# Kernel tuning notes

Measured on AMD Instinct MI355X. Metric: run time of the kernel, lower is better.

The kernel has to match this reference:

```python
import jax, jax.numpy as jnp
import numpy as np

S, B, E, H = 2048, 2, 1024, 16
D = E // H  # head_dim = 64


def setup_inputs() -> dict:
    key = jax.random.key(0)
    ks = jax.random.split(key, 5)
    sp = (2.0 / (E + E)) ** 0.5  # xavier-ish scale
    return {
        "x": jax.random.normal(ks[0], (S, B, E), dtype=jnp.float32),
        "wq": jax.random.normal(ks[1], (E, E), dtype=jnp.float32) * sp,
        "bq": jnp.zeros((E,), jnp.float32),
        "wk": jax.random.normal(ks[2], (E, E), dtype=jnp.float32) * sp,
        "bk": jnp.zeros((E,), jnp.float32),
        "wv": jax.random.normal(ks[3], (E, E), dtype=jnp.float32) * sp,
        "bv": jnp.zeros((E,), jnp.float32),
        "wo": jax.random.normal(ks[4], (E, E), dtype=jnp.float32) * sp,
        "bo": jnp.zeros((E,), jnp.float32),
    }


def reference(x, wq, bq, wk, bk, wv, bv, wo, bo):
    # x: (S, B, E), weights in torch Linear convention (out, in)
    scaling = jnp.float32(D ** -0.5)
    q = (jnp.einsum('ibe,fe->ibf', x, wq) + bq) * scaling
    k = jnp.einsum('ibe,fe->ibf', x, wk) + bk
    v = jnp.einsum('ibe,fe->ibf', x, wv) + bv
    q = q.reshape(S, B, H, D)
    k = k.reshape(S, B, H, D)
    v = v.reshape(S, B, H, D)
    # energy: (B, H, S_q, S_k)
    energy = jnp.einsum('ibnf,jbnf->bnij', q, k)
    causal = jnp.triu(jnp.ones((S, S), dtype=bool), k=1)  # True above diagonal
    energy = jnp.where(causal[None, None], -jnp.inf, energy)
    weights = jax.nn.softmax(energy, axis=-1)
    head_ctx = jnp.einsum('bnij,jbnf->ibnf', weights, v)
    context = head_ctx.reshape(S, B, E)
    out = jnp.einsum('ibe,fe->ibf', context, wo) + bo
    return out
```

## Files before the change

### kernel.cpp

```cpp
#include <hip/hip_runtime.h>
#include <hip/hip_bf16.h>
#include <stdint.h>

#define S_LEN 2048
#define BATCH 2
#define EMB   1024
#define NH    16
#define HD    64
#define LOG2E 1.4426950408889634f

typedef __bf16 bf16x8 __attribute__((ext_vector_type(8)));
typedef float  f32x4  __attribute__((ext_vector_type(4)));
typedef unsigned short ushort8 __attribute__((ext_vector_type(8)));

__device__ __forceinline__ unsigned short f2bf(float f) {
  __bf16 h = (__bf16)f;
  return __builtin_bit_cast(unsigned short, h);
}

__device__ __forceinline__ ushort8 cvt8(const float4 a, const float4 b) {
  ushort8 o;
  o[0]=f2bf(a.x); o[1]=f2bf(a.y); o[2]=f2bf(a.z); o[3]=f2bf(a.w);
  o[4]=f2bf(b.x); o[5]=f2bf(b.y); o[6]=f2bf(b.z); o[7]=f2bf(b.w);
  return o;
}

#define GLOAD16(g, l) __builtin_amdgcn_global_load_lds( \
    (const __attribute__((address_space(1))) void*)(g),  \
    (__attribute__((address_space(3))) void*)(l), 16, 0, 0)

__global__ __launch_bounds__(256) void k_cvt(const float* __restrict__ src,
                                             unsigned short* __restrict__ dst,
                                             int n) {
  int i = (blockIdx.x*256 + threadIdx.x)*8;
  if (i >= n) return;
  const float4* s4 = (const float4*)(src + i);
  *(ushort8*)(dst + i) = cvt8(s4[0], s4[1]);
}

__global__ __launch_bounds__(256) void k_qkv_bb(
    const unsigned short* __restrict__ xb,
    const unsigned short* __restrict__ wb,
    const float* __restrict__ bq, const float* __restrict__ bk,
    const float* __restrict__ bv,
    unsigned short* __restrict__ Qb, unsigned short* __restrict__ Kb,
    unsigned short* __restrict__ Vtb)
{
  __shared__ unsigned short Al[128*32];
  __shared__ unsigned short Bl[128*32];
  const int tid = threadIdx.x;
  const int lin  = blockIdx.x;
  const int wgid = (lin & 7)*96 + (lin >> 3);
  const int mb   = wgid / 24;
  const int t    = wgid % 24;
  const int z    = t >> 3;
  const int nb   = t & 7;
  const int m0 = mb * 128;
  const int n0 = nb * 128;
  const int w = tid >> 6, lane = tid & 63;
  const int wr = w >> 1, wc = w & 1;
  const int lr = lane & 15, lhi = lane >> 4;
  const unsigned short* wz = wb + (size_t)z * (EMB*EMB);

  f32x4 acc[4][4];
#pragma unroll
  for (int m=0;m<4;++m)
#pragma unroll
    for (int n=0;n<4;++n) acc[m][n] = (f32x4){0.f,0.f,0.f,0.f};

  for (int k0 = 0; k0 < EMB; k0 += 32) {
    __syncthreads();
#pragma unroll
    for (int j = 0; j < 2; ++j) {
      const int c   = j*256 + tid;
      const int row = c >> 2;
      const int col = (c & 3) << 3;
      const int ub  = (j*256 + (tid & 192)) * 16;
      GLOAD16(xb + (size_t)(m0+row)*EMB + k0 + col, (char*)Al + ub);
      GLOAD16(wz + (size_t)(n0+row)*EMB + k0 + col, (char*)Bl + ub);
    }
    __syncthreads();
    bf16x8 af[4], bfr[4];
#pragma unroll
    for (int m=0;m<4;++m) af[m]  = *(const bf16x8*)&Al[(wr*64 + m*16 + lr)*32 + lhi*8];
#pragma unroll
    for (int n=0;n<4;++n) bfr[n] = *(const bf16x8*)&Bl[(wc*64 + n*16 + lr)*32 + lhi*8];
#pragma unroll
    for (int m=0;m<4;++m)
#pragma unroll
      for (int n=0;n<4;++n)
        acc[m][n] = __builtin_amdgcn_mfma_f32_16x16x32_bf16(af[m], bfr[n], acc[m][n], 0,0,0);
  }

  const float scale = (z==0) ? 0.125f*LOG2E : 1.0f;
  const float* bias = (z==0) ? bq : ((z==1) ? bk : bv);
#pragma unroll
  for (int m=0;m<4;++m)
#pragma unroll
    for (int n=0;n<4;++n)
#pragma unroll
      for (int r=0;r<4;++r) {
        const int rr   = m0 + wr*64 + m*16 + lhi*4 + r;
        const int fcol = n0 + wc*64 + n*16 + lr;
        const float v = (acc[m][n][r] + bias[fcol]) * scale;
        const unsigned short ov = f2bf(v);
        const int i = rr >> 1, bsel = rr & 1;
        const int h = fcol >> 6, d = fcol & 63;
        const int hh = bsel*NH + h;
        if (z == 0)      Qb [((size_t)hh*S_LEN + i)*HD + d] = ov;
        else if (z == 1) Kb [((size_t)hh*S_LEN + i)*HD + d] = ov;
        else             Vtb[((size_t)hh*HD + d)*S_LEN + i] = ov;
      }
}

__global__ __launch_bounds__(256) void k_qkv_bf(
    const unsigned short* __restrict__ xb,
    const float* __restrict__ wq, const float* __restrict__ wk,
    const float* __restrict__ wv,
    const float* __restrict__ bq, const float* __restrict__ bk,
    const float* __restrict__ bv,
    unsigned short* __restrict__ Qb, unsigned short* __restrict__ Kb,
    unsigned short* __restrict__ Vtb)
{
  __shared__ unsigned short Al[128*32];
  __shared__ unsigned short Bl[128*32];
  const int tid = threadIdx.x;
  const int lin  = blockIdx.x;
  const int wgid = (lin & 7)*96 + (lin >> 3);
  const int mb   = wgid / 24;
  const int t    = wgid % 24;
  const int z    = t >> 3;
  const int nb   = t & 7;
  const int m0 = mb * 128;
  const int n0 = nb * 128;
  const int w = tid >> 6, lane = tid & 63;
  const int wr = w >> 1, wc = w & 1;
  const int lr = lane & 15, lhi = lane >> 4;
  const float* wz = (z==0) ? wq : ((z==1) ? wk : wv);

  f32x4 acc[4][4];
#pragma unroll
  for (int m=0;m<4;++m)
#pragma unroll
    for (int n=0;n<4;++n) acc[m][n] = (f32x4){0.f,0.f,0.f,0.f};

  for (int k0 = 0; k0 < EMB; k0 += 32) {
    float4 b0[2], b1[2];
#pragma unroll
    for (int j = 0; j < 2; ++j) {
      const int c   = j*256 + tid;
      const int row = c >> 2;
      const int col = (c & 3) << 3;
      const float* bp = wz + (size_t)(n0+row)*EMB + k0 + col;
      b0[j] = *(const float4*)bp;  b1[j] = *(const float4*)(bp+4);
    }
    __syncthreads();
#pragma unroll
    for (int j = 0; j < 2; ++j) {
      const int c   = j*256 + tid;
      const int row = c >> 2;
      const int col = (c & 3) << 3;
      const int ub  = (j*256 + (tid & 192)) * 16;
      GLOAD16(xb + (size_t)(m0+row)*EMB + k0 + col, (char*)Al + ub);
      *(ushort8*)&Bl[row*32 + col] = cvt8(b0[j], b1[j]);
    }
    __syncthreads();
    bf16x8 af[4], bfr[4];
#pragma unroll
    for (int m=0;m<4;++m) af[m]  = *(const bf16x8*)&Al[(wr*64 + m*16 + lr)*32 + lhi*8];
#pragma unroll
    for (int n=0;n<4;++n) bfr[n] = *(const bf16x8*)&Bl[(wc*64 + n*16 + lr)*32 + lhi*8];
#pragma unroll
    for (int m=0;m<4;++m)
#pragma unroll
      for (int n=0;n<4;++n)
        acc[m][n] = __builtin_amdgcn_mfma_f32_16x16x32_bf16(af[m], bfr[n], acc[m][n], 0,0,0);
  }

  const float scale = (z==0) ? 0.125f*LOG2E : 1.0f;
  const float* bias = (z==0) ? bq : ((z==1) ? bk : bv);
#pragma unroll
  for (int m=0;m<4;++m)
#pragma unroll
    for (int n=0;n<4;++n)
#pragma unroll
      for (int r=0;r<4;++r) {
        const int rr   = m0 + wr*64 + m*16 + lhi*4 + r;
        const int fcol = n0 + wc*64 + n*16 + lr;
        const float v = (acc[m][n][r] + bias[fcol]) * scale;
        const unsigned short ov = f2bf(v);
        const int i = rr >> 1, bsel = rr & 1;
        const int h = fcol >> 6, d = fcol & 63;
        const int hh = bsel*NH + h;
        if (z == 0)      Qb [((size_t)hh*S_LEN + i)*HD + d] = ov;
        else if (z == 1) Kb [((size_t)hh*S_LEN + i)*HD + d] = ov;
        else             Vtb[((size_t)hh*HD + d)*S_LEN + i] = ov;
      }
}

__global__ __launch_bounds__(256) void k_qkv(
    const float* __restrict__ xA, int a_rs, int ishift,
    const float* __restrict__ wq, const float* __restrict__ wk,
    const float* __restrict__ wv,
    const float* __restrict__ bq, const float* __restrict__ bk,
    const float* __restrict__ bv,
    unsigned short* __restrict__ Qb, unsigned short* __restrict__ Kb,
    unsigned short* __restrict__ Vtb)
{
  __shared__ unsigned short Al[128*32];
  __shared__ unsigned short Bl[128*32];
  const int tid = threadIdx.x;
  const int z  = blockIdx.z;
  const int m0 = blockIdx.x * 128;
  const int n0 = blockIdx.y * 128;
  const int w = tid >> 6, lane = tid & 63;
  const int wr = w >> 1, wc = w & 1;
  const int lr = lane & 15, lhi = lane >> 4;
  const float* wz = (z==0) ? wq : ((z==1) ? wk : wv);

  f32x4 acc[4][4];
#pragma unroll
  for (int m=0;m<4;++m)
#pragma unroll
    for (int n=0;n<4;++n) acc[m][n] = (f32x4){0.f,0.f,0.f,0.f};

  for (int k0 = 0; k0 < EMB; k0 += 32) {
    float4 a0[2], a1[2], b0[2], b1[2];
#pragma unroll
    for (int j = 0; j < 2; ++j) {
      const int c   = j*256 + tid;
      const int row = c >> 2;
      const int col = (c & 3) << 3;
      const float* ap = xA + (size_t)(m0+row)*a_rs + k0 + col;
      const float* bp = wz + (size_t)(n0+row)*EMB + k0 + col;
      a0[j] = *(const float4*)ap;  a1[j] = *(const float4*)(ap+4);
      b0[j] = *(const float4*)bp;  b1[j] = *(const float4*)(bp+4);
    }
    __syncthreads();
#pragma unroll
    for (int j = 0; j < 2; ++j) {
      const int c   = j*256 + tid;
      const int row = c >> 2;
      const int col = (c & 3) << 3;
      *(ushort8*)&Al[row*32 + col] = cvt8(a0[j], a1[j]);
      *(ushort8*)&Bl[row*32 + col] = cvt8(b0[j], b1[j]);
    }
    __syncthreads();
    bf16x8 af[4], bfr[4];
#pragma unroll
    for (int m=0;m<4;++m) af[m]  = *(const bf16x8*)&Al[(wr*64 + m*16 + lr)*32 + lhi*8];
#pragma unroll
    for (int n=0;n<4;++n) bfr[n] = *(const bf16x8*)&Bl[(wc*64 + n*16 + lr)*32 + lhi*8];
#pragma unroll
    for (int m=0;m<4;++m)
#pragma unroll
      for (int n=0;n<4;++n)
        acc[m][n] = __builtin_amdgcn_mfma_f32_16x16x32_bf16(af[m], bfr[n], acc[m][n], 0,0,0);
  }

  const float scale = (z==0) ? 0.125f*LOG2E : 1.0f;
  const float* bias = (z==0) ? bq : ((z==1) ? bk : bv);
  const int bmask = (1 << ishift) - 1;
#pragma unroll
  for (int m=0;m<4;++m)
#pragma unroll
    for (int n=0;n<4;++n)
#pragma unroll
      for (int r=0;r<4;++r) {
        const int rr   = m0 + wr*64 + m*16 + lhi*4 + r;
        const int fcol = n0 + wc*64 + n*16 + lr;
        const float v = (acc[m][n][r] + bias[fcol]) * scale;
        const unsigned short ov = f2bf(v);
        const int i = rr >> ishift, bsel = rr & bmask;
        const int h = fcol >> 6, d = fcol & 63;
        const int hh = bsel*NH + h;
        if (z == 0)      Qb [((size_t)hh*S_LEN + i)*HD + d] = ov;
        else if (z == 1) Kb [((size_t)hh*S_LEN + i)*HD + d] = ov;
        else             Vtb[((size_t)hh*HD + d)*S_LEN + i] = ov;
      }
}

__global__ __launch_bounds__(256,4) void k_attn(
    const unsigned short* __restrict__ Q,
    const unsigned short* __restrict__ K,
    const unsigned short* __restrict__ Vt,
    unsigned short* __restrict__ ctx, int bshift, int hsh)
{
  __shared__ unsigned short KL[2][64*64];
  __shared__ unsigned short VL[2][64*64];
  __shared__ unsigned short Pl[4][1024];

  const int tid = threadIdx.x;
  const int w = tid >> 6, lane = tid & 63;
  const int lr = lane & 15, lhi = lane >> 4;

  const int lin = blockIdx.x;
  const int cc  = lin >> hsh;
  const int chunk = (cc < 16) ? cc : (47 - cc);
  const int hh  = lin & ((1 << hsh) - 1);
  const int q0  = chunk*64 + w*16;

  const unsigned short* Qh = Q  + (size_t)hh*S_LEN*HD;
  const unsigned short* Kh = K  + (size_t)hh*S_LEN*HD;
  const unsigned short* Vh = Vt + (size_t)hh*HD*S_LEN;
  unsigned short* Pw = Pl[w];

  bf16x8 qf[2];
#pragma unroll
  for (int kf=0;kf<2;++kf)
    qf[kf] = *(const bf16x8*)&Qh[(size_t)(q0 + lr)*HD + kf*32 + lhi*8];

  f32x4 o[4];
  float rm = -3.0e38f, rl = 0.f;
#pragma unroll
  for (int dn=0;dn<4;++dn) o[dn] = (f32x4){0.f,0.f,0.f,0.f};

  const int tmax = chunk + 1;

  auto STAGE = [&](int tt, int bb2) {
    const int kv0 = tt*64;
#pragma unroll
    for (int j = 0; j < 2; ++j) {
      const int c   = j*256 + tid;
      const int row = c >> 3;
      const int sb  = (c*16) ^ ((row & 7) << 4);
      const int el  = (sb & 127) >> 1;
      const int ub  = (j*256 + (tid & 192)) * 16;
      GLOAD16(Kh + (size_t)(kv0+row)*HD + el,        (char*)KL[bb2] + ub);
      GLOAD16(Vh + (size_t)row*S_LEN + kv0 + el,     (char*)VL[bb2] + ub);
    }
  };

  STAGE(0, 0);
  int bb = 0;
  for (int t = 0; t < tmax; ++t) {
    if (t + 1 < tmax) {
      STAGE(t+1, bb^1);
      asm volatile("s_waitcnt vmcnt(4)" ::: "memory");
    } else {
      asm volatile("s_waitcnt vmcnt(0)" ::: "memory");
    }
    __builtin_amdgcn_s_barrier();

    const int kv0 = t*64;
    const char* KB = (const char*)KL[bb];
    const char* VB = (const char*)VL[bb];

    f32x4 st[4];
#pragma unroll
    for (int kn=0;kn<4;++kn) st[kn] = (f32x4){0.f,0.f,0.f,0.f};

    __builtin_amdgcn_s_setprio(1);
#pragma unroll
    for (int kn=0;kn<4;++kn)
#pragma unroll
      for (int kf=0;kf<2;++kf) {
        const int row = kn*16 + lr;
        const int byt = ((row<<7) + kf*64 + lhi*16) ^ ((row & 7) << 4);
        const bf16x8 kfr = *(const bf16x8*)(KB + byt);
        st[kn] = __builtin_amdgcn_mfma_f32_16x16x32_bf16(kfr, qf[kf], st[kn], 0,0,0);
      }
    __builtin_amdgcn_s_setprio(0);

    if (t == tmax-1) {
      const int q = q0 + lr;
#pragma unroll
      for (int kn=0;kn<4;++kn)
#pragma unroll
        for (int r=0;r<4;++r) {
          const int k = kv0 + kn*16 + lhi*4 + r;
          if (k > q) st[kn][r] = -1.0e30f;
        }
    }

    float mx = fmaxf(fmaxf(st[0][0], st[0][1]), fmaxf(st[0][2], st[0][3]));
#pragma unroll
    for (int kn=1;kn<4;++kn)
      mx = fmaxf(mx, fmaxf(fmaxf(st[kn][0], st[kn][1]),
                           fmaxf(st[kn][2], st[kn][3])));
    mx = fmaxf(mx, __shfl_xor(mx, 16));
    mx = fmaxf(mx, __shfl_xor(mx, 32));
    if (!__all(mx - rm <= 8.0f)) {
      const float newm  = fmaxf(rm, mx);
      const float alpha = exp2f(rm - newm);
      rl *= alpha;
#pragma unroll
      for (int dn=0;dn<4;++dn)
#pragma unroll
        for (int r=0;r<4;++r) o[dn][r] *= alpha;
      rm = newm;
    }
    float sum = 0.f;
#pragma unroll
    for (int kn=0;kn<4;++kn)
#pragma unroll
      for (int r=0;r<4;++r) {
        const float p = exp2f(st[kn][r] - rm);
        st[kn][r] = p;
        sum += p;
      }
    sum += __shfl_xor(sum, 16);
    sum += __shfl_xor(sum, 32);
    rl += sum;

    {
      const int qrow = lr;
#pragma unroll
      for (int kn=0;kn<4;++kn) {
        unsigned long long pk =
            (unsigned long long)f2bf(st[kn][0])
          | ((unsigned long long)f2bf(st[kn][1]) << 16)
          | ((unsigned long long)f2bf(st[kn][2]) << 32)
          | ((unsigned long long)f2bf(st[kn][3]) << 48);
        const int byt = (qrow*128 + kn*32 + lhi*8) ^ ((qrow & 7) << 4);
        *(unsigned long long*)((char*)Pw + byt) = pk;
      }
    }

#pragma unroll
    for (int ks=0;ks<2;++ks) {
      const int qrow = lr;
      const int pby = (qrow*128 + ks*64 + lhi*16) ^ ((qrow & 7) << 4);
      const bf16x8 pfr = *(const bf16x8*)((char*)Pw + pby);
      __builtin_amdgcn_s_setprio(1);
#pragma unroll
      for (int dn=0;dn<4;++dn) {
        const int row = dn*16 + lr;
        const int byt = ((row<<7) + ks*64 + lhi*16) ^ ((row & 7) << 4);
        const bf16x8 vf = *(const bf16x8*)(VB + byt);
        o[dn] = __builtin_amdgcn_mfma_f32_16x16x32_bf16(vf, pfr, o[dn], 0,0,0);
      }
      __builtin_amdgcn_s_setprio(0);
    }

    __builtin_amdgcn_s_barrier();
    bb ^= 1;
  }

  const int h = hh & (NH-1);
  const int badd = hh >> 4;
  const float inv = 1.0f / rl;
  const int q = q0 + lr;
  const size_t trow = ((size_t)q << bshift) + badd;
#pragma unroll
  for (int dn=0;dn<4;++dn) {
    unsigned long long pk =
        (unsigned long long)f2bf(o[dn][0]*inv)
      | ((unsigned long long)f2bf(o[dn][1]*inv) << 16)
      | ((unsigned long long)f2bf(o[dn][2]*inv) << 32)
      | ((unsigned long long)f2bf(o[dn][3]*inv) << 48);
    *(unsigned long long*)&ctx[trow*EMB + h*HD + dn*16 + lhi*4] = pk;
  }
}

__global__ __launch_bounds__(256) void k_oproj_bf(
    const unsigned short* __restrict__ ctxA,
    const unsigned short* __restrict__ wob,
    const float* __restrict__ bo,
    float* __restrict__ out)
{
  __shared__ unsigned short Al[128*32];
  __shared__ unsigned short Bl[128*32];
  const int tid = threadIdx.x;
  const int m0 = blockIdx.x * 128;
  const int n0 = blockIdx.y * 128;
  const int w = tid >> 6, lane = tid & 63;
  const int wr = w >> 1, wc = w & 1;
  const int lr = lane & 15, lhi = lane >> 4;

  f32x4 acc[4][4];
#pragma unroll
  for (int m=0;m<4;++m)
#pragma unroll
    for (int n=0;n<4;++n) acc[m][n] = (f32x4){0.f,0.f,0.f,0.f};

  for (int k0 = 0; k0 < EMB; k0 += 32) {
    __syncthreads();
#pragma unroll
    for (int j = 0; j < 2; ++j) {
      const int c   = j*256 + tid;
      const int row = c >> 2;
      const int col = (c & 3) << 3;
      const int ub  = (j*256 + (tid & 192)) * 16;
      GLOAD16(ctxA + (size_t)(m0+row)*EMB + k0 + col, (char*)Al + ub);
      GLOAD16(wob  + (size_t)(n0+row)*EMB + k0 + col, (char*)Bl + ub);
    }
    __syncthreads();
    bf16x8 af[4], bfr[4];
#pragma unroll
    for (int m=0;m<4;++m) af[m]  = *(const bf16x8*)&Al[(wr*64 + m*16 + lr)*32 + lhi*8];
#pragma unroll
    for (int n=0;n<4;++n) bfr[n] = *(const bf16x8*)&Bl[(wc*64 + n*16 + lr)*32 + lhi*8];
#pragma unroll
    for (int m=0;m<4;++m)
#pragma unroll
      for (int n=0;n<4;++n)
        acc[m][n] = __builtin_amdgcn_mfma_f32_16x16x32_bf16(af[m], bfr[n], acc[m][n], 0,0,0);
  }

#pragma unroll
  for (int m=0;m<4;++m)
#pragma unroll
    for (int n=0;n<4;++n)
#pragma unroll
      for (int r=0;r<4;++r) {
        const int rr   = m0 + wr*64 + m*16 + lhi*4 + r;
        const int fcol = n0 + wc*64 + n*16 + lr;
        out[(size_t)rr*EMB + fcol] = acc[m][n][r] + bo[fcol];
      }
}

__global__ __launch_bounds__(256) void k_oproj(
    const unsigned short* __restrict__ ctxA,
    const float* __restrict__ wo,
    const float* __restrict__ bo,
    float* __restrict__ outb, int orm)
{
  __shared__ unsigned short Al[128*32];
  __shared__ unsigned short Bl[128*32];
  const int tid = threadIdx.x;
  const int m0 = blockIdx.x * 128;
  const int n0 = blockIdx.y * 128;
  const int w = tid >> 6, lane = tid & 63;
  const int wr = w >> 1, wc = w & 1;
  const int lr = lane & 15, lhi = lane >> 4;

  f32x4 acc[4][4];
#pragma unroll
  for (int m=0;m<4;++m)
#pragma unroll
    for (int n=0;n<4;++n) acc[m][n] = (f32x4){0.f,0.f,0.f,0.f};

  for (int k0 = 0; k0 < EMB; k0 += 32) {
    float4 b0[2], b1[2];
#pragma unroll
    for (int j = 0; j < 2; ++j) {
      const int c   = j*256 + tid;
      const int row = c >> 2;
      const int col = (c & 3) << 3;
      const float* bp = wo + (size_t)(n0+row)*EMB + k0 + col;
      b0[j] = *(const float4*)bp;  b1[j] = *(const float4*)(bp+4);
    }
    __syncthreads();
#pragma unroll
    for (int j = 0; j < 2; ++j) {
      const int c   = j*256 + tid;
      const int row = c >> 2;
      const int col = (c & 3) << 3;
      const int ub  = (j*256 + (tid & 192)) * 16;
      GLOAD16(ctxA + (size_t)(m0+row)*EMB + k0 + col, (char*)Al + ub);
      *(ushort8*)&Bl[row*32 + col] = cvt8(b0[j], b1[j]);
    }
    __syncthreads();
    bf16x8 af[4], bfr[4];
#pragma unroll
    for (int m=0;m<4;++m) af[m]  = *(const bf16x8*)&Al[(wr*64 + m*16 + lr)*32 + lhi*8];
#pragma unroll
    for (int n=0;n<4;++n) bfr[n] = *(const bf16x8*)&Bl[(wc*64 + n*16 + lr)*32 + lhi*8];
#pragma unroll
    for (int m=0;m<4;++m)
#pragma unroll
      for (int n=0;n<4;++n)
        acc[m][n] = __builtin_amdgcn_mfma_f32_16x16x32_bf16(af[m], bfr[n], acc[m][n], 0,0,0);
  }

#pragma unroll
  for (int m=0;m<4;++m)
#pragma unroll
    for (int n=0;n<4;++n)
#pragma unroll
      for (int r=0;r<4;++r) {
        const int rr   = m0 + wr*64 + m*16 + lhi*4 + r;
        const int fcol = n0 + wc*64 + n*16 + lr;
        outb[(size_t)rr*orm*EMB + fcol] = acc[m][n][r] + bo[fcol];
      }
}

extern "C" void kernel_launch(void* const* d_in, const int* in_sizes, int n_in,
                              void* d_out, int out_size, void* d_ws, size_t ws_size,
                              hipStream_t stream) {
  const float* x  = (const float*)d_in[0];
  const float* wq = (const float*)d_in[1];
  const float* bq = (const float*)d_in[2];
  const float* wk = (const float*)d_in[3];
  const float* bk = (const float*)d_in[4];
  const float* wv = (const float*)d_in[5];
  const float* bv = (const float*)d_in[6];
  const float* wo = (const float*)d_in[7];
  const float* bo = (const float*)d_in[8];
  float* out = (float*)d_out;

  char* ws = (char*)d_ws;
  const size_t MB = (size_t)1 << 20;

  if (ws_size >= 38*MB) {
    unsigned short* Q   = (unsigned short*)(ws + 0*MB);
    unsigned short* K   = (unsigned short*)(ws + 8*MB);
    unsigned short* Vt  = (unsigned short*)(ws + 16*MB);
    unsigned short* wb  = (unsigned short*)(ws + 24*MB);
    unsigned short* xb  = (unsigned short*)(ws + 30*MB);
    unsigned short* cx  = (unsigned short*)(ws + 24*MB);
    unsigned short* wob = Vt;

    k_cvt<<<2048, 256, 0, stream>>>(x,  xb, (S_LEN*BATCH)*EMB);
    k_cvt<<<512,  256, 0, stream>>>(wq, wb + (size_t)0*EMB*EMB, EMB*EMB);
    k_cvt<<<512,  256, 0, stream>>>(wk, wb + (size_t)1*EMB*EMB, EMB*EMB);
    k_cvt<<<512,  256, 0, stream>>>(wv, wb + (size_t)2*EMB*EMB, EMB*EMB);
    k_qkv_bb<<<768, 256, 0, stream>>>(xb, wb, bq,bk,bv, Q, K, Vt);
    k_attn<<<1024, 256, 0, stream>>>(Q, K, Vt, cx, 1, 5);
    k_cvt<<<512, 256, 0, stream>>>(wo, wob, EMB*EMB);
    k_oproj_bf<<<dim3(32,8), 256, 0, stream>>>(cx, wob, bo, out);
  } else if (ws_size >= 32*MB) {
    unsigned short* Q   = (unsigned short*)(ws + 0*MB);
    unsigned short* K   = (unsigned short*)(ws + 8*MB);
    unsigned short* Vt  = (unsigned short*)(ws + 16*MB);
    unsigned short* cx  = (unsigned short*)(ws + 24*MB);
    unsigned short* xb  = cx;
    unsigned short* wob = Vt;

    k_cvt<<<2048, 256, 0, stream>>>(x, xb, (S_LEN*BATCH)*EMB);
    k_qkv_bf<<<768, 256, 0, stream>>>(xb, wq,wk,wv, bq,bk,bv, Q, K, Vt);
    k_attn<<<1024, 256, 0, stream>>>(Q, K, Vt, cx, 1, 5);
    k_cvt<<<512, 256, 0, stream>>>(wo, wob, EMB*EMB);
    k_oproj_bf<<<dim3(32,8), 256, 0, stream>>>(cx, wob, bo, out);
  } else {
    unsigned short* Q  = (unsigned short*)(ws + 0*MB);
    unsigned short* K  = (unsigned short*)(ws + 4*MB);
    unsigned short* Vt = (unsigned short*)(ws + 8*MB);
    unsigned short* cx = (unsigned short*)(ws + 12*MB);
    for (int b = 0; b < 2; ++b) {
      k_qkv<<<dim3(16,8,3), 256, 0, stream>>>(x + b*EMB, 2*EMB, 0,
                                              wq,wk,wv, bq,bk,bv, Q,K,Vt);
      k_attn<<<512, 256, 0, stream>>>(Q, K, Vt, cx, 0, 4);
      k_oproj<<<dim3(16,8), 256, 0, stream>>>(cx, wo, bo, out + b*EMB, 2);
    }
  }
}
```

Measured before the change: 131.7 us.

## Widen attention query tile to 128 rows with two 16-row sub-tiles per wave

The attention kernel now processes 128 query rows per block (32 per wave, as two 16-row MFMA sub-tiles), so each K/V fragment loaded from LDS feeds two MFMAs and each staged K/V tile is shared by twice as many queries. The grid is halved, causal chunk pairing is adjusted, and waves skip compute on tiles beyond their own causal limit while still joining the barriers. LDS and global address offsets are precomputed. The cost is more registers and lower occupancy (launch bounds lowered to 3), fewer blocks, and idle waves on diagonal tiles.

Result: slower. 147.2 us (+11.7%).

```diff
diff --git a/kernel.cpp b/kernel.cpp
--- a/kernel.cpp
+++ b/kernel.cpp
@@ -23,6 +23,13 @@
   o[0]=f2bf(a.x); o[1]=f2bf(a.y); o[2]=f2bf(a.z); o[3]=f2bf(a.w);
   o[4]=f2bf(b.x); o[5]=f2bf(b.y); o[6]=f2bf(b.z); o[7]=f2bf(b.w);
   return o;
+}
+
+__device__ __forceinline__ unsigned long long pack4(const f32x4 v) {
+  return  (unsigned long long)f2bf(v[0])
+       | ((unsigned long long)f2bf(v[1]) << 16)
+       | ((unsigned long long)f2bf(v[2]) << 32)
+       | ((unsigned long long)f2bf(v[3]) << 48);
 }
 
 #define GLOAD16(g, l) __builtin_amdgcn_global_load_lds( \
@@ -280,7 +287,7 @@
       }
 }
 
-__global__ __launch_bounds__(256,4) void k_attn(
+__global__ __launch_bounds__(256,3) void k_attn(
     const unsigned short* __restrict__ Q,
     const unsigned short* __restrict__ K,
     const unsigned short* __restrict__ Vt,
@@ -288,7 +295,7 @@
 {
   __shared__ unsigned short KL[2][64*64];
   __shared__ unsigned short VL[2][64*64];
-  __shared__ unsigned short Pl[4][1024];
+  __shared__ unsigned short Pl[4][32*64];
 
   const int tid = threadIdx.x;
   const int w = tid >> 6, lane = tid & 63;
@@ -296,38 +303,62 @@
 
   const int lin = blockIdx.x;
   const int cc  = lin >> hsh;
-  const int chunk = (cc < 16) ? cc : (47 - cc);
+  const int chunk = (cc < 8) ? cc : (23 - cc);
   const int hh  = lin & ((1 << hsh) - 1);
-  const int q0  = chunk*64 + w*16;
+  const int q0  = chunk*128 + w*32;
 
   const unsigned short* Qh = Q  + (size_t)hh*S_LEN*HD;
   const unsigned short* Kh = K  + (size_t)hh*S_LEN*HD;
   const unsigned short* Vh = Vt + (size_t)hh*HD*S_LEN;
-  unsigned short* Pw = Pl[w];
-
-  bf16x8 qf[2];
-#pragma unroll
-  for (int kf=0;kf<2;++kf)
-    qf[kf] = *(const bf16x8*)&Qh[(size_t)(q0 + lr)*HD + kf*32 + lhi*8];
-
-  f32x4 o[4];
-  float rm = -3.0e38f, rl = 0.f;
-#pragma unroll
-  for (int dn=0;dn<4;++dn) o[dn] = (f32x4){0.f,0.f,0.f,0.f};
-
-  const int tmax = chunk + 1;
+  char* Pw = (char*)Pl[w];
+
+  const int xm = (lr & 7) << 4;
+  int kvb[2];
+#pragma unroll
+  for (int kf=0;kf<2;++kf) kvb[kf] = lr*128 + ((kf*64 + lhi*16) ^ xm);
+  int pwb[2][4];
+#pragma unroll
+  for (int qm=0;qm<2;++qm)
+#pragma unroll
+    for (int kn=0;kn<4;++kn)
+      pwb[qm][kn] = qm*2048 + lr*128 + ((kn*32 + lhi*8) ^ xm);
+
+  const unsigned short* kga[2];
+  const unsigned short* vga[2];
+#pragma unroll
+  for (int j=0;j<2;++j) {
+    const int c   = j*256 + tid;
+    const int row = c >> 3;
+    const int sb  = (c*16) ^ ((row & 7) << 4);
+    const int el  = (sb & 127) >> 1;
+    kga[j] = Kh + (size_t)row*HD + el;
+    vga[j] = Vh + (size_t)row*S_LEN + el;
+  }
+  const int ub0 = (tid & 192) * 16;
+
+  bf16x8 qf[2][2];
+#pragma unroll
+  for (int qm=0;qm<2;++qm)
+#pragma unroll
+    for (int kf=0;kf<2;++kf)
+      qf[qm][kf] = *(const bf16x8*)&Qh[(size_t)(q0 + qm*16 + lr)*HD + kf*32 + lhi*8];
+
+  f32x4 o[4][2];
+  float rm[2], rl[2];
+#pragma unroll
+  for (int dn=0;dn<4;++dn)
+#pragma unroll
+    for (int qm=0;qm<2;++qm) o[dn][qm] = (f32x4){0.f,0.f,0.f,0.f};
+  rm[0] = rm[1] = -3.0e38f;  rl[0] = rl[1] = 0.f;
+
+  const int wtend = ((q0 + 31) >> 6) + 1;
+  const int tmax  = 2*chunk + 2;
 
   auto STAGE = [&](int tt, int bb2) {
-    const int kv0 = tt*64;
-#pragma unroll
-    for (int j = 0; j < 2; ++j) {
-      const int c   = j*256 + tid;
-      const int row = c >> 3;
-      const int sb  = (c*16) ^ ((row & 7) << 4);
-      const int el  = (sb & 127) >> 1;
-      const int ub  = (j*256 + (tid & 192)) * 16;
-      GLOAD16(Kh + (size_t)(kv0+row)*HD + el,        (char*)KL[bb2] + ub);
-      GLOAD16(Vh + (size_t)row*S_LEN + kv0 + el,     (char*)VL[bb2] + ub);
+#pragma unroll
+    for (int j=0;j<2;++j) {
+      GLOAD16(kga[j] + (size_t)tt*4096, (char*)KL[bb2] + ub0 + j*4096);
+      GLOAD16(vga[j] + (size_t)tt*64,   (char*)VL[bb2] + ub0 + j*4096);
     }
   };
 
@@ -342,114 +373,126 @@
     }
     __builtin_amdgcn_s_barrier();
 
-    const int kv0 = t*64;
-    const char* KB = (const char*)KL[bb];
-    const char* VB = (const char*)VL[bb];
-
-    f32x4 st[4];
-#pragma unroll
-    for (int kn=0;kn<4;++kn) st[kn] = (f32x4){0.f,0.f,0.f,0.f};
-
-    __builtin_amdgcn_s_setprio(1);
-#pragma unroll
-    for (int kn=0;kn<4;++kn)
-#pragma unroll
-      for (int kf=0;kf<2;++kf) {
-        const int row = kn*16 + lr;
-        const int byt = ((row<<7) + kf*64 + lhi*16) ^ ((row & 7) << 4);
-        const bf16x8 kfr = *(const bf16x8*)(KB + byt);
-        st[kn] = __builtin_amdgcn_mfma_f32_16x16x32_bf16(kfr, qf[kf], st[kn], 0,0,0);
-      }
-    __builtin_amdgcn_s_setprio(0);
-
-    if (t == tmax-1) {
-      const int q = q0 + lr;
+    if (t < wtend) {
+      const int kv0 = t*64;
+      const char* KB = (const char*)KL[bb];
+      const char* VB = (const char*)VL[bb];
+
+      f32x4 st[4][2];
 #pragma unroll
       for (int kn=0;kn<4;++kn)
 #pragma unroll
-        for (int r=0;r<4;++r) {
-          const int k = kv0 + kn*16 + lhi*4 + r;
-          if (k > q) st[kn][r] = -1.0e30f;
+        for (int qm=0;qm<2;++qm) st[kn][qm] = (f32x4){0.f,0.f,0.f,0.f};
+
+      __builtin_amdgcn_s_setprio(1);
+#pragma unroll
+      for (int kn=0;kn<4;++kn)
+#pragma unroll
+        for (int kf=0;kf<2;++kf) {
+          const bf16x8 kfr = *(const bf16x8*)(KB + kvb[kf] + kn*2048);
+#pragma unroll
+          for (int qm=0;qm<2;++qm)
+            st[kn][qm] = __builtin_amdgcn_mfma_f32_16x16x32_bf16(kfr, qf[qm][kf], st[kn][qm], 0,0,0);
         }
-    }
-
-    float mx = fmaxf(fmaxf(st[0][0], st[0][1]), fmaxf(st[0][2], st[0][3]));
-#pragma unroll
-    for (int kn=1;kn<4;++kn)
-      mx = fmaxf(mx, fmaxf(fmaxf(st[kn][0], st[kn][1]),
-                           fmaxf(st[kn][2], st[kn][3])));
-    mx = fmaxf(mx, __shfl_xor(mx, 16));
-    mx = fmaxf(mx, __shfl_xor(mx, 32));
-    if (!__all(mx - rm <= 8.0f)) {
-      const float newm  = fmaxf(rm, mx);
-      const float alpha = exp2f(rm - newm);
-      rl *= alpha;
-#pragma unroll
-      for (int dn=0;dn<4;++dn)
-#pragma unroll
-        for (int r=0;r<4;++r) o[dn][r] *= alpha;
-      rm = newm;
-    }
-    float sum = 0.f;
-#pragma unroll
-    for (int kn=0;kn<4;++kn)
-#pragma unroll
-      for (int r=0;r<4;++r) {
-        const float p = exp2f(st[kn][r] - rm);
-        st[kn][r] = p;
-        sum += p;
-      }
-    sum += __shfl_xor(sum, 16);
-    sum += __shfl_xor(sum, 32);
-    rl += sum;
-
-    {
-      const int qrow = lr;
-#pragma unroll
-      for (int kn=0;kn<4;++kn) {
-        unsigned long long pk =
-            (unsigned long long)f2bf(st[kn][0])
-          | ((unsigned long long)f2bf(st[kn][1]) << 16)
-          | ((unsigned long long)f2bf(st[kn][2]) << 32)
-          | ((unsigned long long)f2bf(st[kn][3]) << 48);
-        const int byt = (qrow*128 + kn*32 + lhi*8) ^ ((qrow & 7) << 4);
-        *(unsigned long long*)((char*)Pw + byt) = pk;
-      }
-    }
-
-#pragma unroll
-    for (int ks=0;ks<2;++ks) {
-      const int qrow = lr;
-      const int pby = (qrow*128 + ks*64 + lhi*16) ^ ((qrow & 7) << 4);
-      const bf16x8 pfr = *(const bf16x8*)((char*)Pw + pby);
-      __builtin_amdgcn_s_setprio(1);
-#pragma unroll
-      for (int dn=0;dn<4;++dn) {
-        const int row = dn*16 + lr;
-        const int byt = ((row<<7) + ks*64 + lhi*16) ^ ((row & 7) << 4);
-        const bf16x8 vf = *(const bf16x8*)(VB + byt);
-        o[dn] = __builtin_amdgcn_mfma_f32_16x16x32_bf16(vf, pfr, o[dn], 0,0,0);
-      }
       __builtin_amdgcn_s_setprio(0);
-    }
-
+
+      if (t == wtend-1) {
+#pragma unroll
+        for (int qm=0;qm<2;++qm) {
+          const int q = q0 + qm*16 + lr;
+#pragma unroll
+          for (int kn=0;kn<4;++kn)
+#pragma unroll
+            for (int r=0;r<4;++r) {
+              const int k = kv0 + kn*16 + lhi*4 + r;
+              if (k > q) st[kn][qm][r] = -1.0e30f;
+            }
+        }
+      }
+
+      float mx[2];
+#pragma unroll
+      for (int qm=0;qm<2;++qm) {
+        float m_ = fmaxf(fmaxf(st[0][qm][0], st[0][qm][1]),
+                         fmaxf(st[0][qm][2], st[0][qm][3]));
+#pragma unroll
+        for (int kn=1;kn<4;++kn)
+          m_ = fmaxf(m_, fmaxf(fmaxf(st[kn][qm][0], st[kn][qm][1]),
+                               fmaxf(st[kn][qm][2], st[kn][qm][3])));
+        m_ = fmaxf(m_, __shfl_xor(m_, 16));
+        m_ = fmaxf(m_, __shfl_xor(m_, 32));
+        mx[qm] = m_;
+      }
+      if (!__all(fmaxf(mx[0]-rm[0], mx[1]-rm[1]) <= 8.0f)) {
+#pragma unroll
+        for (int qm=0;qm<2;++qm) {
+          const float newm  = fmaxf(rm[qm], mx[qm]);
+          const float alpha = exp2f(rm[qm] - newm);
+          rl[qm] *= alpha;
+#pragma unroll
+          for (int dn=0;dn<4;++dn)
+#pragma unroll
+            for (int r=0;r<4;++r) o[dn][qm][r] *= alpha;
+          rm[qm] = newm;
+        }
+      }
+#pragma unroll
+      for (int qm=0;qm<2;++qm) {
+        float sum = 0.f;
+#pragma unroll
+        for (int kn=0;kn<4;++kn)
+#pragma unroll
+          for (int r=0;r<4;++r) {
+            const float p = exp2f(st[kn][qm][r] - rm[qm]);
+            st[kn][qm][r] = p;
+            sum += p;
+          }
+        sum += __shfl_xor(sum, 16);
+        sum += __shfl_xor(sum, 32);
+        rl[qm] += sum;
+      }
+
+#pragma unroll
+      for (int qm=0;qm<2;++qm)
+#pragma unroll
+        for (int kn=0;kn<4;++kn)
+          *(unsigned long long*)(Pw + pwb[qm][kn]) = pack4(st[kn][qm]);
+
+#pragma unroll
+      for (int ks=0;ks<2;++ks) {
+        bf16x8 pfr[2];
+#pragma unroll
+        for (int qm=0;qm<2;++qm)
+          pfr[qm] = *(const bf16x8*)(Pw + kvb[ks] + qm*2048);
+        __builtin_amdgcn_s_setprio(1);
+#pragma unroll
+        for (int dn=0;dn<4;++dn) {
+          const bf16x8 vf = *(const bf16x8*)(VB + kvb[ks] + dn*2048);
+#pragma unroll
+          for (int qm=0;qm<2;++qm)
+            o[dn][qm] = __builtin_amdgcn_mfma_f32_16x16x32_bf16(vf, pfr[qm], o[dn][qm], 0,0,0);
+        }
+        __builtin_amdgcn_s_setprio(0);
+      }
+    }
     __builtin_amdgcn_s_barrier();
     bb ^= 1;
   }
 
   const int h = hh & (NH-1);
   const int badd = hh >> 4;
-  const float inv = 1.0f / rl;
-  const int q = q0 + lr;
-  const size_t trow = ((size_t)q << bshift) + badd;
-#pragma unroll
-  for (int dn=0;dn<4;++dn) {
-    unsigned long long pk =
-        (unsigned long long)f2bf(o[dn][0]*inv)
-      | ((unsigned long long)f2bf(o[dn][1]*inv) << 16)
-      | ((unsigned long long)f2bf(o[dn][2]*inv) << 32)
-      | ((unsigned long long)f2bf(o[dn][3]*inv) << 48);
-    *(unsigned long long*)&ctx[trow*EMB + h*HD + dn*16 + lhi*4] = pk;
+#pragma unroll
+  for (int qm=0;qm<2;++qm) {
+    const float inv = 1.0f / rl[qm];
+    const int q = q0 + qm*16 + lr;
+    const size_t trow = ((size_t)q << bshift) + badd;
+#pragma unroll
+    for (int dn=0;dn<4;++dn) {
+      f32x4 ov;
+#pragma unroll
+      for (int r=0;r<4;++r) ov[r] = o[dn][qm][r]*inv;
+      *(unsigned long long*)&ctx[trow*EMB + h*HD + dn*16 + lhi*4] = pack4(ov);
+    }
   }
 }
 
@@ -607,7 +650,7 @@
     k_cvt<<<512,  256, 0, stream>>>(wk, wb + (size_t)1*EMB*EMB, EMB*EMB);
     k_cvt<<<512,  256, 0, stream>>>(wv, wb + (size_t)2*EMB*EMB, EMB*EMB);
     k_qkv_bb<<<768, 256, 0, stream>>>(xb, wb, bq,bk,bv, Q, K, Vt);
-    k_attn<<<1024, 256, 0, stream>>>(Q, K, Vt, cx, 1, 5);
+    k_attn<<<512, 256, 0, stream>>>(Q, K, Vt, cx, 1, 5);
     k_cvt<<<512, 256, 0, stream>>>(wo, wob, EMB*EMB);
     k_oproj_bf<<<dim3(32,8), 256, 0, stream>>>(cx, wob, bo, out);
   } else if (ws_size >= 32*MB) {
@@ -620,7 +663,7 @@
 
     k_cvt<<<2048, 256, 0, stream>>>(x, xb, (S_LEN*BATCH)*EMB);
     k_qkv_bf<<<768, 256, 0, stream>>>(xb, wq,wk,wv, bq,bk,bv, Q, K, Vt);
-    k_attn<<<1024, 256, 0, stream>>>(Q, K, Vt, cx, 1, 5);
+    k_attn<<<512, 256, 0, stream>>>(Q, K, Vt, cx, 1, 5);
     k_cvt<<<512, 256, 0, stream>>>(wo, wob, EMB*EMB);
     k_oproj_bf<<<dim3(32,8), 256, 0, stream>>>(cx, wob, bo, out);
   } else {
@@ -631,7 +674,7 @@
     for (int b = 0; b < 2; ++b) {
       k_qkv<<<dim3(16,8,3), 256, 0, stream>>>(x + b*EMB, 2*EMB, 0,
                                               wq,wk,wv, bq,bk,bv, Q,K,Vt);
-      k_attn<<<512, 256, 0, stream>>>(Q, K, Vt, cx, 0, 4);
+      k_attn<<<256, 256, 0, stream>>>(Q, K, Vt, cx, 0, 4);
       k_oproj<<<dim3(16,8), 256, 0, stream>>>(cx, wo, bo, out + b*EMB, 2);
     }
   }
```
